# Kernel optimization log

Measured on AMD Instinct MI355X. Metric: run time of the kernel, lower is better.

Reference implementation:

```python
import jax, jax.numpy as jnp
import numpy as np

B, N = 256, 131072

def setup_inputs() -> dict:
    key = jax.random.key(0)
    kx, km = jax.random.split(key)
    x = jax.random.normal(kx, (B, N), dtype=jnp.float32)
    mask = jax.random.randint(km, (B, N), 0, 2).astype(jnp.bool_)
    return {"x": x, "mask": mask}

def reference(x, mask):
    # Masked cumulative sum along dim=1: zero out masked-off entries, then scan.
    return jnp.cumsum(jnp.where(mask, x, 0.0), axis=1)
```

## Files before the change

### kernel.cpp

```cpp
#include <hip/hip_runtime.h>


#define N_ROWS   256
#define N_COLS   131072
#define BLOCK    1024
#define VPT      16
#define NV4      (VPT / 4)
#define TILE     (BLOCK * VPT)
#define NTILES   (N_COLS / TILE)
#define NWAVES   (BLOCK / 64)

__global__ __launch_bounds__(BLOCK, 4)
void masked_cumsum_kernel(const float* __restrict__ x,
                          const int* __restrict__ mask,
                          float* __restrict__ out) {
    __shared__ float waveSums[2][NWAVES];

    const int tid  = threadIdx.x;
    const int lane = tid & 63;
    const int wave = tid >> 6;

    const size_t rowBase = (size_t)blockIdx.x * N_COLS;
    const float4* __restrict__ x4 = (const float4*)(x + rowBase);
    const int4*   __restrict__ m4 = (const int4*)(mask + rowBase);
    float4*       __restrict__ o4 = (float4*)(out + rowBase);

    float carry = 0.0f;

    float4 xa[NV4];
    int4   ma[NV4];
    #pragma unroll
    for (int k = 0; k < NV4; ++k) {
        xa[k] = x4[tid * NV4 + k];
        ma[k] = m4[tid * NV4 + k];
    }

    for (int t = 0; t < NTILES; ++t) {
        float s[VPT];
        float run = 0.0f;
        #pragma unroll
        for (int k = 0; k < NV4; ++k) {
            run += ma[k].x ? xa[k].x : 0.0f; s[4*k+0] = run;
            run += ma[k].y ? xa[k].y : 0.0f; s[4*k+1] = run;
            run += ma[k].z ? xa[k].z : 0.0f; s[4*k+2] = run;
            run += ma[k].w ? xa[k].w : 0.0f; s[4*k+3] = run;
        }
        const float tsum = run;

        if (t + 1 < NTILES) {
            const int nb = (t + 1) * BLOCK * NV4 + tid * NV4;
            #pragma unroll
            for (int k = 0; k < NV4; ++k) {
                xa[k] = x4[nb + k];
                ma[k] = m4[nb + k];
            }
        }

        float incl = tsum;
        #pragma unroll
        for (int d = 1; d < 64; d <<= 1) {
            const float y = __shfl_up(incl, d, 64);
            if (lane >= d) incl += y;
        }
        const float waveExcl = incl - tsum;

        if (lane == 63) waveSums[t & 1][wave] = incl;
        __syncthreads();

        float waveOff = 0.0f, tileTot = 0.0f;
        #pragma unroll
        for (int w = 0; w < NWAVES; ++w) {
            const float v = waveSums[t & 1][w];
            if (w < wave) waveOff += v;
            tileTot += v;
        }

        const float base = carry + waveOff + waveExcl;
        const int ob = t * BLOCK * NV4 + tid * NV4;
        #pragma unroll
        for (int k = 0; k < NV4; ++k) {
            float4 r;
            r.x = base + s[4*k+0];
            r.y = base + s[4*k+1];
            r.z = base + s[4*k+2];
            r.w = base + s[4*k+3];
            o4[ob + k] = r;
        }

        carry += tileTot;
    }
}

extern "C" void kernel_launch(void* const* d_in, const int* in_sizes, int n_in,
                              void* d_out, int out_size, void* d_ws, size_t ws_size,
                              hipStream_t stream) {
    const float* x    = (const float*)d_in[0];
    const int*   mask = (const int*)d_in[1];
    float*       out  = (float*)d_out;
    (void)in_sizes; (void)n_in; (void)out_size; (void)d_ws; (void)ws_size;

    masked_cumsum_kernel<<<N_ROWS, BLOCK, 0, stream>>>(x, mask, out);
}
```

Before: 319.6 us.

## Split rows into chunks with decoupled look-back scan across blocks

Replaces one block per row, which loops serially over tiles, with 4096 blocks that each handle a 8192-element chunk. Blocks take a dynamic ticket so chunk order is preserved, publish their aggregate or inclusive prefix as packed flags, and use a wave-wide look-back over earlier chunks to get their exclusive offset. This raises parallelism beyond 256 blocks to fill the GPU and hide memory latency. In exchange it adds a workspace memset, atomic traffic and spin-waiting on flags.

```diff
diff --git a/kernel.cpp b/kernel.cpp
--- a/kernel.cpp
+++ b/kernel.cpp
@@ -3,29 +3,47 @@
 
 #define N_ROWS   256
 #define N_COLS   131072
-#define BLOCK    1024
+#define BLOCK    512
 #define VPT      16
 #define NV4      (VPT / 4)
-#define TILE     (BLOCK * VPT)
-#define NTILES   (N_COLS / TILE)
+#define PART     (BLOCK * VPT)
+#define PPR      (N_COLS / PART)
+#define NBLOCKS  (N_ROWS * PPR)
 #define NWAVES   (BLOCK / 64)
 
-__global__ __launch_bounds__(BLOCK, 4)
-void masked_cumsum_kernel(const float* __restrict__ x,
-                          const int* __restrict__ mask,
-                          float* __restrict__ out) {
-    __shared__ float waveSums[2][NWAVES];
+#define WS_TICKET_OFF 0
+#define WS_FLAGS_OFF  64
+#define WS_BYTES      (WS_FLAGS_OFF + NBLOCKS * 8)
+
+__device__ __forceinline__ unsigned long long pack_desc(unsigned long long flag, float v) {
+    union { float f; unsigned u; } c; c.f = v;
+    return (flag << 32) | (unsigned long long)c.u;
+}
+
+__global__ __launch_bounds__(BLOCK)
+void masked_cumsum_lookback(const float* __restrict__ x,
+                            const int* __restrict__ mask,
+                            float* __restrict__ out,
+                            unsigned int* __restrict__ ticket,
+                            unsigned long long* __restrict__ flags) {
+    __shared__ float waveSums[NWAVES];
+    __shared__ float s_excl;
+    __shared__ unsigned int s_vid;
 
     const int tid  = threadIdx.x;
     const int lane = tid & 63;
     const int wave = tid >> 6;
 
-    const size_t rowBase = (size_t)blockIdx.x * N_COLS;
-    const float4* __restrict__ x4 = (const float4*)(x + rowBase);
-    const int4*   __restrict__ m4 = (const int4*)(mask + rowBase);
-    float4*       __restrict__ o4 = (float4*)(out + rowBase);
+    if (tid == 0) s_vid = atomicAdd(ticket, 1u);
+    __syncthreads();
+    const unsigned vid = s_vid;
+    const int row  = (int)(vid >> 4);
+    const int part = (int)(vid & (PPR - 1));
 
-    float carry = 0.0f;
+    const size_t gbase = (size_t)row * N_COLS + (size_t)part * PART;
+    const float4* __restrict__ x4 = (const float4*)(x + gbase);
+    const int4*   __restrict__ m4 = (const int4*)(mask + gbase);
+    float4*       __restrict__ o4 = (float4*)(out + gbase);
 
     float4 xa[NV4];
     int4   ma[NV4];
@@ -35,59 +53,92 @@
         ma[k] = m4[tid * NV4 + k];
     }
 
-    for (int t = 0; t < NTILES; ++t) {
-        float s[VPT];
-        float run = 0.0f;
-        #pragma unroll
-        for (int k = 0; k < NV4; ++k) {
-            run += ma[k].x ? xa[k].x : 0.0f; s[4*k+0] = run;
-            run += ma[k].y ? xa[k].y : 0.0f; s[4*k+1] = run;
-            run += ma[k].z ? xa[k].z : 0.0f; s[4*k+2] = run;
-            run += ma[k].w ? xa[k].w : 0.0f; s[4*k+3] = run;
-        }
-        const float tsum = run;
+    float s[VPT];
+    float run = 0.0f;
+    #pragma unroll
+    for (int k = 0; k < NV4; ++k) {
+        run += ma[k].x ? xa[k].x : 0.0f; s[4*k+0] = run;
+        run += ma[k].y ? xa[k].y : 0.0f; s[4*k+1] = run;
+        run += ma[k].z ? xa[k].z : 0.0f; s[4*k+2] = run;
+        run += ma[k].w ? xa[k].w : 0.0f; s[4*k+3] = run;
+    }
+    const float tsum = run;
 
-        if (t + 1 < NTILES) {
-            const int nb = (t + 1) * BLOCK * NV4 + tid * NV4;
-            #pragma unroll
-            for (int k = 0; k < NV4; ++k) {
-                xa[k] = x4[nb + k];
-                ma[k] = m4[nb + k];
+    float incl = tsum;
+    #pragma unroll
+    for (int d = 1; d < 64; d <<= 1) {
+        const float y = __shfl_up(incl, d, 64);
+        if (lane >= d) incl += y;
+    }
+    const float waveExcl = incl - tsum;
+
+    if (lane == 63) waveSums[wave] = incl;
+    __syncthreads();
+
+    float waveOff = 0.0f, blockTot = 0.0f;
+    #pragma unroll
+    for (int w = 0; w < NWAVES; ++w) {
+        const float v = waveSums[w];
+        if (w < wave) waveOff += v;
+        blockTot += v;
+    }
+
+    if (wave == 0) {
+        if (part == 0) {
+            if (lane == 0) {
+                __hip_atomic_store(&flags[vid], pack_desc(2ull, blockTot),
+                                   __ATOMIC_RELEASE, __HIP_MEMORY_SCOPE_AGENT);
+                s_excl = 0.0f;
+            }
+        } else {
+            if (lane == 0) {
+                __hip_atomic_store(&flags[vid], pack_desc(1ull, blockTot),
+                                   __ATOMIC_RELEASE, __HIP_MEMORY_SCOPE_AGENT);
+            }
+            const unsigned long long* fr = flags + ((size_t)row << 4);
+            float excl = 0.0f;
+            for (;;) {
+                int   flg = 2;
+                float val = 0.0f;
+                if (lane < part) {
+                    const unsigned long long e =
+                        __hip_atomic_load(&fr[part - 1 - lane],
+                                          __ATOMIC_ACQUIRE, __HIP_MEMORY_SCOPE_AGENT);
+                    flg = (int)(e >> 32);
+                    union { unsigned u; float f; } c;
+                    c.u = (unsigned)(e & 0xffffffffu);
+                    val = c.f;
+                }
+                if (__ballot(flg == 0) != 0ull) {
+                    __builtin_amdgcn_s_sleep(1);
+                    continue;
+                }
+                const unsigned long long pfx = __ballot(flg == 2);
+                const int istar = __ffsll((long long)pfx) - 1;
+                float c = (lane <= istar) ? val : 0.0f;
+                #pragma unroll
+                for (int m = 1; m < 64; m <<= 1) c += __shfl_xor(c, m, 64);
+                excl = c;
+                break;
+            }
+            if (lane == 0) {
+                __hip_atomic_store(&flags[vid], pack_desc(2ull, excl + blockTot),
+                                   __ATOMIC_RELEASE, __HIP_MEMORY_SCOPE_AGENT);
+                s_excl = excl;
             }
         }
+    }
+    __syncthreads();
 
-        float incl = tsum;
-        #pragma unroll
-        for (int d = 1; d < 64; d <<= 1) {
-            const float y = __shfl_up(incl, d, 64);
-            if (lane >= d) incl += y;
-        }
-        const float waveExcl = incl - tsum;
-
-        if (lane == 63) waveSums[t & 1][wave] = incl;
-        __syncthreads();
-
-        float waveOff = 0.0f, tileTot = 0.0f;
-        #pragma unroll
-        for (int w = 0; w < NWAVES; ++w) {
-            const float v = waveSums[t & 1][w];
-            if (w < wave) waveOff += v;
-            tileTot += v;
-        }
-
-        const float base = carry + waveOff + waveExcl;
-        const int ob = t * BLOCK * NV4 + tid * NV4;
-        #pragma unroll
-        for (int k = 0; k < NV4; ++k) {
-            float4 r;
-            r.x = base + s[4*k+0];
-            r.y = base + s[4*k+1];
-            r.z = base + s[4*k+2];
-            r.w = base + s[4*k+3];
-            o4[ob + k] = r;
-        }
-
-        carry += tileTot;
+    const float basev = s_excl + waveOff + waveExcl;
+    #pragma unroll
+    for (int k = 0; k < NV4; ++k) {
+        float4 r;
+        r.x = basev + s[4*k+0];
+        r.y = basev + s[4*k+1];
+        r.z = basev + s[4*k+2];
+        r.w = basev + s[4*k+3];
+        o4[tid * NV4 + k] = r;
     }
 }
 
@@ -97,7 +148,12 @@
     const float* x    = (const float*)d_in[0];
     const int*   mask = (const int*)d_in[1];
     float*       out  = (float*)d_out;
-    (void)in_sizes; (void)n_in; (void)out_size; (void)d_ws; (void)ws_size;
+    (void)in_sizes; (void)n_in; (void)out_size; (void)ws_size;
 
-    masked_cumsum_kernel<<<N_ROWS, BLOCK, 0, stream>>>(x, mask, out);
+    unsigned int* ticket = (unsigned int*)((char*)d_ws + WS_TICKET_OFF);
+    unsigned long long* flags = (unsigned long long*)((char*)d_ws + WS_FLAGS_OFF);
+
+    hipMemsetAsync(d_ws, 0, WS_BYTES, stream);
+
+    masked_cumsum_lookback<<<NBLOCKS, BLOCK, 0, stream>>>(x, mask, out, ticket, flags);
 }
```

After: 928.2 us. +190.5%, slower.
